# Optimization experiments

Hardware: AMD Instinct MI355X
Metric: run time of the kernel (lower is better)

## Reference

```python
import jax, jax.numpy as jnp
import numpy as np

L, E, K, H, I = 2, 8, 2, 1024, 2048  # stack_size, num_experts, top_k, hidden, intermediate
B, S = 1, 2048


def setup_inputs() -> dict:
    key = jax.random.key(0)
    k0, k1, k2, k3 = jax.random.split(key, 4)
    hidden_states = jax.random.normal(k0, (B, S, H), dtype=jnp.float32)
    router_w = jax.random.normal(k1, (L, H, E), dtype=jnp.float32) * 0.02
    gate_up_proj = jax.random.normal(k2, (L, E, H, 2 * I), dtype=jnp.float32) * (1.0 / np.sqrt(H))
    down_proj = jax.random.normal(k3, (L, E, I, H), dtype=jnp.float32) * (1.0 / np.sqrt(I))
    return {"hidden_states": hidden_states, "router_w": router_w,
            "gate_up_proj": gate_up_proj, "down_proj": down_proj}


def _moe_layer(x, rw, gu_w, dn_w):
    # x: [T,H]; one MoE block: RouterTopK(softmax) + full-capacity top-k GLU expert MLPs
    logits = x @ rw                                   # [T,E] router linear (fp32)
    aff = jax.nn.softmax(logits, axis=-1)
    vals, idx = jax.lax.top_k(aff, K)                 # [T,K]
    vals = vals / jnp.sum(vals, axis=-1, keepdims=True)  # normalize_top_k_affinities=True
    T = x.shape[0]
    # sparse combine weights [T,E]: normalized affinity on chosen experts, 0 elsewhere
    combine = jnp.zeros((T, E), x.dtype).at[jnp.arange(T)[:, None], idx].set(vals)
    gu = jnp.einsum('th,ehi->eti', x, gu_w)           # [E,T,2I] fused gate+up per expert
    gate, up = gu[..., :I], gu[..., I:]
    act = jax.nn.silu(gate) * up                      # GLU with silu
    eo = jnp.einsum('eti,eih->eth', act, dn_w)        # [E,T,H] down proj
    out = jnp.einsum('eth,te->th', eo, combine)       # combine over experts
    return out, logits


def reference(hidden_states, router_w, gate_up_proj, down_proj):
    Bx, Sx, Hx = hidden_states.shape
    x = hidden_states.reshape(-1, Hx)                 # [T,H]
    logits_all = []
    for l in range(L):                                # fixed small stack of layers
        x, logits = _moe_layer(x, router_w[l], gate_up_proj[l], down_proj[l])
        logits_all.append(logits)
    return x.reshape(Bx, Sx, Hx), jnp.stack(logits_all)  # output, [L,T,E] router logits
```

## Files before the change

kernel.cpp:

```cpp
#include <hip/hip_runtime.h>
#include <cstdint>
#include <cstddef>

constexpr int Lc = 2, Ec = 8, Hc = 1024, Ic = 2048, Tc = 2048;

typedef __bf16 bf16x8 __attribute__((ext_vector_type(8)));
typedef float f32x4 __attribute__((ext_vector_type(4)));

__device__ __forceinline__ unsigned short f2bf(float f) {
  unsigned u = __builtin_bit_cast(unsigned, f);
  u = (u + 0x7fffu + ((u >> 16) & 1u)) >> 16;
  return (unsigned short)u;
}
__device__ __forceinline__ float bf2f(unsigned short h) {
  unsigned u = (unsigned)h << 16;
  return __builtin_bit_cast(float, u);
}
__device__ __forceinline__ bf16x8 ldfrag(const unsigned short* p) {
  return __builtin_bit_cast(bf16x8, *(const uint4*)p);
}
__device__ __forceinline__ void gl2lds(const unsigned short* g, void* lds) {
  __builtin_amdgcn_global_load_lds(
      (const __attribute__((address_space(1))) void*)g,
      (__attribute__((address_space(3))) void*)lds, 16, 0, 0);
}

__global__ __launch_bounds__(256) void router_kernel(
    const float* __restrict__ x, const float* __restrict__ rw, float* __restrict__ logits,
    unsigned short* __restrict__ xh, unsigned short* __restrict__ xl) {
  const int t = blockIdx.x;
  const int tid = threadIdx.x;
  const float* xr = x + (size_t)t * Hc;
  const int h0 = tid * 4;
  const float4 v = *(const float4*)(xr + h0);
  const float f[4] = {v.x, v.y, v.z, v.w};
  unsigned short hs[4], ls[4];
#pragma unroll
  for (int j = 0; j < 4; ++j) {
    hs[j] = f2bf(f[j]);
    ls[j] = f2bf(f[j] - bf2f(hs[j]));
  }
  *(uint2*)(xh + (size_t)t * Hc + h0) =
      uint2{(unsigned)hs[0] | ((unsigned)hs[1] << 16), (unsigned)hs[2] | ((unsigned)hs[3] << 16)};
  *(uint2*)(xl + (size_t)t * Hc + h0) =
      uint2{(unsigned)ls[0] | ((unsigned)ls[1] << 16), (unsigned)ls[2] | ((unsigned)ls[3] << 16)};

  float acc[Ec];
#pragma unroll
  for (int e = 0; e < Ec; ++e) acc[e] = 0.f;
#pragma unroll
  for (int j = 0; j < 4; ++j) {
    const float* w = rw + (size_t)(h0 + j) * Ec;
#pragma unroll
    for (int e = 0; e < Ec; ++e) acc[e] += f[j] * w[e];
  }
  __shared__ float red[256][Ec];
#pragma unroll
  for (int e = 0; e < Ec; ++e) red[tid][e] = acc[e];
  __syncthreads();
  for (int s = 128; s > 0; s >>= 1) {
    if (tid < s) {
#pragma unroll
      for (int e = 0; e < Ec; ++e) red[tid][e] += red[tid + s][e];
    }
    __syncthreads();
  }
  if (tid < Ec) logits[(size_t)t * Ec + tid] = red[0][tid];
}

__global__ void topk_kernel(const float* __restrict__ logits, int* __restrict__ cnt,
                            int* __restrict__ tokList, float* __restrict__ wList) {
  const int t = blockIdx.x * blockDim.x + threadIdx.x;
  if (t >= Tc) return;
  float l[Ec];
#pragma unroll
  for (int e = 0; e < Ec; ++e) l[e] = logits[(size_t)t * Ec + e];
  float b0 = -3.4e38f, b1 = -3.4e38f;
  int i0 = 0, i1 = 0;
#pragma unroll
  for (int e = 0; e < Ec; ++e) {
    if (l[e] > b0) { b1 = b0; i1 = i0; b0 = l[e]; i0 = e; }
    else if (l[e] > b1) { b1 = l[e]; i1 = e; }
  }
  const float w0 = 1.f / (1.f + expf(b1 - b0));
  const float w1 = 1.f - w0;
  int p0 = atomicAdd(&cnt[i0], 1);
  tokList[i0 * Tc + p0] = t;
  wList[i0 * Tc + p0] = w0;
  int p1 = atomicAdd(&cnt[i1], 1);
  tokList[i1 * Tc + p1] = t;
  wList[i1 * Tc + p1] = w1;
}

__global__ void offsets_kernel(const int* __restrict__ cnt, int* __restrict__ off) {
  if (threadIdx.x == 0) {
    int s = 0;
    for (int e = 0; e < Ec; ++e) { off[e] = s; s += cnt[e]; }
  }
}

template <bool SPLIT>
__global__ __launch_bounds__(256) void wconv_kernel(const float* __restrict__ src,
                                                    unsigned short* __restrict__ dh,
                                                    unsigned short* __restrict__ dl,
                                                    int K, int N) {
  const int e = blockIdx.z;
  const int n0 = blockIdx.x * 64;
  const int k0 = blockIdx.y * 64;
  const int NB = N >> 6, KS = K >> 5;
  src += (size_t)e * K * N;

  __shared__ unsigned short lh[64][66];
  __shared__ unsigned short ll[SPLIT ? 64 : 1][66];
  const int tid = threadIdx.x;

  {
    const int r = tid >> 2, cg = (tid & 3) * 16;
    const float* sp = src + (size_t)(k0 + r) * N + n0 + cg;
#pragma unroll
    for (int i = 0; i < 16; i += 4) {
      const float4 v = *(const float4*)(sp + i);
      const float f[4] = {v.x, v.y, v.z, v.w};
#pragma unroll
      for (int j = 0; j < 4; ++j) {
        const unsigned short h = f2bf(f[j]);
        lh[r][cg + i + j] = h;
        if constexpr (SPLIT) ll[r][cg + i + j] = f2bf(f[j] - bf2f(h));
      }
    }
  }
  __syncthreads();
  {
    const int ksl = tid >> 7, q = (tid >> 5) & 3, n2 = (tid & 31) * 2;
    const int kb = ksl * 32 + q * 8;
    union { unsigned short s[16]; uint4 u[2]; } oh, ol;
#pragma unroll
    for (int s = 0; s < 2; ++s)
#pragma unroll
      for (int i = 0; i < 8; ++i) {
        oh.s[s * 8 + i] = lh[kb + i][n2 + s];
        if constexpr (SPLIT) ol.s[s * 8 + i] = ll[kb + i][n2 + s];
      }
    const size_t cb =
        (((size_t)e * NB + (n0 >> 6)) * KS + (k0 >> 5) + ksl) * 2048 + q * 512 + n2 * 8;
    *(uint4*)(dh + cb) = oh.u[0];
    *(uint4*)(dh + cb + 8) = oh.u[1];
    if constexpr (SPLIT) {
      *(uint4*)(dl + cb) = ol.u[0];
      *(uint4*)(dl + cb + 8) = ol.u[1];
    }
  }
}

template <bool SPLIT>
__global__ __launch_bounds__(256) void gateup_kernel(
    const unsigned short* __restrict__ xh, const unsigned short* __restrict__ xl,
    const unsigned short* __restrict__ gwSh, const unsigned short* __restrict__ gwSl,
    const int* __restrict__ cnt, const int* __restrict__ off,
    const int* __restrict__ tokList, unsigned short* __restrict__ actH,
    unsigned short* __restrict__ actL) {
  const int d = blockIdx.x;
  const int lid = (d & 7) * ((int)gridDim.x >> 3) + (d >> 3);
  const int mi = lid & 15;
  const int e = (lid >> 4) & 7;
  const int nb = lid >> 7;
  const int M = cnt[e];
  const int m0 = mi * 128;
  if (m0 >= M) return;
  const int tid = threadIdx.x;
  const int wv = tid >> 6, l64 = tid & 63;
  const int q = l64 >> 4, mr = l64 & 15;
  const int nc = wv * 16 + mr;
  const int wvo = wv * 1024;

  __shared__ __align__(16) unsigned short sBgh[3][2048];
  __shared__ __align__(16) unsigned short sBgl[3][SPLIT ? 2048 : 8];
  __shared__ __align__(16) unsigned short sBuh[3][2048];
  __shared__ __align__(16) unsigned short sBul[3][SPLIT ? 2048 : 8];
  __shared__ __align__(16) unsigned short sAh[2][128 * 40];
  __shared__ __align__(16) unsigned short sAl[2][SPLIT ? 128 * 40 : 8];

  const size_t gBase = (((size_t)e * 64 + nb) * 32) * 2048 + tid * 8;
  const size_t uBase = (((size_t)e * 64 + nb + 32) * 32) * 2048 + tid * 8;

  const int ar = tid >> 2, ak = (tid & 3) * 8;
  int r0 = m0 + ar;      if (r0 >= M) r0 = M - 1;
  int r1 = m0 + 64 + ar; if (r1 >= M) r1 = M - 1;
  const size_t a0o = (size_t)tokList[e * Tc + r0] * Hc + ak;
  const size_t a1o = (size_t)tokList[e * Tc + r1] * Hc + ak;

  f32x4 accg[8], accu[8];
#pragma unroll
  for (int i = 0; i < 8; ++i) {
    accg[i] = f32x4{0.f, 0.f, 0.f, 0.f};
    accu[i] = f32x4{0.f, 0.f, 0.f, 0.f};
  }

  uint4 pa0h{}, pa1h{}, pa0l{}, pa1l{};
  uint4 pb0h{}, pb1h{}, pb0l{}, pb1l{};

  pa0h = *(const uint4*)(xh + a0o);
  pa1h = *(const uint4*)(xh + a1o);
  if constexpr (SPLIT) {
    pa0l = *(const uint4*)(xl + a0o);
    pa1l = *(const uint4*)(xl + a1o);
  }
  gl2lds(gwSh + gBase, (char*)sBgh[0] + wvo);
  gl2lds(gwSh + uBase, (char*)sBuh[0] + wvo);
  if constexpr (SPLIT) {
    gl2lds(gwSl + gBase, (char*)sBgl[0] + wvo);
    gl2lds(gwSl + uBase, (char*)sBul[0] + wvo);
  }
  *(uint4*)&sAh[0][ar * 40 + ak] = pa0h;
  *(uint4*)&sAh[0][(ar + 64) * 40 + ak] = pa1h;
  if constexpr (SPLIT) {
    *(uint4*)&sAl[0][ar * 40 + ak] = pa0l;
    *(uint4*)&sAl[0][(ar + 64) * 40 + ak] = pa1l;
  }
  pa0h = *(const uint4*)(xh + a0o + 32);
  pa1h = *(const uint4*)(xh + a1o + 32);
  if constexpr (SPLIT) {
    pa0l = *(const uint4*)(xl + a0o + 32);
    pa1l = *(const uint4*)(xl + a1o + 32);
  }
  gl2lds(gwSh + gBase + 2048, (char*)sBgh[1] + wvo);
  gl2lds(gwSh + uBase + 2048, (char*)sBuh[1] + wvo);
  if constexpr (SPLIT) {
    gl2lds(gwSl + gBase + 2048, (char*)sBgl[1] + wvo);
    gl2lds(gwSl + uBase + 2048, (char*)sBul[1] + wvo);
  }
  if constexpr (SPLIT)
    asm volatile("s_waitcnt vmcnt(8) lgkmcnt(0)" ::: "memory");
  else
    asm volatile("s_waitcnt vmcnt(4) lgkmcnt(0)" ::: "memory");
  __builtin_amdgcn_s_barrier();
  __builtin_amdgcn_sched_barrier(0);

  int cbuf = 0, ibuf = 2;

#define GU_STEP(T, RB, WB, O0H, O1H, O0L, O1L, N0H, N1H, N0L, N1L)                      \
  {                                                                                     \
    if ((T) + 2 < 32) {                                                                 \
      N0H = *(const uint4*)(xh + a0o + ((T) + 2) * 32);                                 \
      N1H = *(const uint4*)(xh + a1o + ((T) + 2) * 32);                                 \
      if constexpr (SPLIT) {                                                            \
        N0L = *(const uint4*)(xl + a0o + ((T) + 2) * 32);                               \
        N1L = *(const uint4*)(xl + a1o + ((T) + 2) * 32);                               \
      }                                                                                 \
      gl2lds(gwSh + gBase + (size_t)((T) + 2) * 2048, (char*)sBgh[ibuf] + wvo);         \
      gl2lds(gwSh + uBase + (size_t)((T) + 2) * 2048, (char*)sBuh[ibuf] + wvo);         \
      if constexpr (SPLIT) {                                                            \
        gl2lds(gwSl + gBase + (size_t)((T) + 2) * 2048, (char*)sBgl[ibuf] + wvo);       \
        gl2lds(gwSl + uBase + (size_t)((T) + 2) * 2048, (char*)sBul[ibuf] + wvo);       \
      }                                                                                 \
    }                                                                                   \
    if ((T) + 1 < 32) {                                                                 \
      *(uint4*)&sAh[WB][ar * 40 + ak] = O0H;                                            \
      *(uint4*)&sAh[WB][(ar + 64) * 40 + ak] = O1H;                                     \
      if constexpr (SPLIT) {                                                            \
        *(uint4*)&sAl[WB][ar * 40 + ak] = O0L;                                          \
        *(uint4*)&sAl[WB][(ar + 64) * 40 + ak] = O1L;                                   \
      }                                                                                 \
    }                                                                                   \
    const bf16x8 bghf = ldfrag(&sBgh[cbuf][(q * 64 + nc) * 8]);                         \
    const bf16x8 buhf = ldfrag(&sBuh[cbuf][(q * 64 + nc) * 8]);                         \
    bf16x8 bglf, bulf;                                                                  \
    if constexpr (SPLIT) {                                                              \
      bglf = ldfrag(&sBgl[cbuf][(q * 64 + nc) * 8]);                                    \
      bulf = ldfrag(&sBul[cbuf][(q * 64 + nc) * 8]);                                    \
    }                                                                                   \
    _Pragma("unroll")                                                                   \
    for (int mt = 0; mt < 8; ++mt) {                                                    \
      const bf16x8 ah = ldfrag(&sAh[RB][(mt * 16 + mr) * 40 + q * 8]);                  \
      accg[mt] = __builtin_amdgcn_mfma_f32_16x16x32_bf16(ah, bghf, accg[mt], 0, 0, 0);  \
      accu[mt] = __builtin_amdgcn_mfma_f32_16x16x32_bf16(ah, buhf, accu[mt], 0, 0, 0);  \
      if constexpr (SPLIT) {                                                            \
        const bf16x8 alr = ldfrag(&sAl[RB][(mt * 16 + mr) * 40 + q * 8]);               \
        accg[mt] = __builtin_amdgcn_mfma_f32_16x16x32_bf16(ah, bglf, accg[mt], 0, 0, 0);\
        accg[mt] = __builtin_amdgcn_mfma_f32_16x16x32_bf16(alr, bghf, accg[mt], 0, 0, 0);\
        accu[mt] = __builtin_amdgcn_mfma_f32_16x16x32_bf16(ah, bulf, accu[mt], 0, 0, 0);\
        accu[mt] = __builtin_amdgcn_mfma_f32_16x16x32_bf16(alr, buhf, accu[mt], 0, 0, 0);\
      }                                                                                 \
    }                                                                                   \
    if ((T) < 31) {                                                                     \
      if ((T) + 2 < 32) {                                                               \
        if constexpr (SPLIT)                                                            \
          asm volatile("s_waitcnt vmcnt(8) lgkmcnt(0)" ::: "memory");                   \
        else                                                                            \
          asm volatile("s_waitcnt vmcnt(4) lgkmcnt(0)" ::: "memory");                   \
      } else {                                                                          \
        asm volatile("s_waitcnt vmcnt(0) lgkmcnt(0)" ::: "memory");                     \
      }                                                                                 \
      __builtin_amdgcn_s_barrier();                                                     \
      __builtin_amdgcn_sched_barrier(0);                                                \
    }                                                                                   \
    cbuf = cbuf == 2 ? 0 : cbuf + 1;                                                    \
    ibuf = ibuf == 2 ? 0 : ibuf + 1;                                                    \
  }

  for (int t = 0; t < 32; t += 2) {
    GU_STEP(t, 0, 1, pa0h, pa1h, pa0l, pa1l, pb0h, pb1h, pb0l, pb1l)
    GU_STEP(t + 1, 1, 0, pb0h, pb1h, pb0l, pb1l, pa0h, pa1h, pa0l, pa1l)
  }
#undef GU_STEP

  const int valid = M - m0;
  const int rowbase = off[e] + m0;
#pragma unroll
  for (int mt = 0; mt < 8; ++mt) {
#pragma unroll
    for (int r = 0; r < 4; ++r) {
      const int row = mt * 16 + q * 4 + r;
      if (row < valid) {
        const float g = accg[mt][r];
        const float u = accu[mt][r];
        const float a = (g / (1.f + expf(-g))) * u;
        const size_t idx = (size_t)(rowbase + row) * Ic + (nb * 64 + nc);
        const unsigned short h = f2bf(a);
        actH[idx] = h;
        if constexpr (SPLIT) actL[idx] = f2bf(a - bf2f(h));
      }
    }
  }
}

template <bool SPLIT>
__global__ __launch_bounds__(256) void down_kernel(
    const unsigned short* __restrict__ actH, const unsigned short* __restrict__ actL,
    const unsigned short* __restrict__ dwSh, const unsigned short* __restrict__ dwSl,
    const int* __restrict__ cnt, const int* __restrict__ off,
    const int* __restrict__ tokList, const float* __restrict__ wList,
    float* __restrict__ out) {
  const int d = blockIdx.x;
  const int lid = (d & 7) * ((int)gridDim.x >> 3) + (d >> 3);
  const int mi = lid & 15;
  const int e = (lid >> 4) & 7;
  const int nb = lid >> 7;
  const int M = cnt[e];
  const int m0 = mi * 128;
  if (m0 >= M) return;
  const int tid = threadIdx.x;
  const int wv = tid >> 6, l64 = tid & 63;
  const int q = l64 >> 4, mr = l64 & 15;
  const int nc = wv * 16 + mr;
  const int wvo = wv * 1024;

  __shared__ __align__(16) unsigned short sBh[3][2048];
  __shared__ __align__(16) unsigned short sBl[3][SPLIT ? 2048 : 8];
  __shared__ __align__(16) unsigned short sAh[2][128 * 40];
  __shared__ __align__(16) unsigned short sAl[2][SPLIT ? 128 * 40 : 8];
  __shared__ int sTok[128];
  __shared__ float sW[128];

  if (tid < 128) {
    int r = m0 + tid;
    int rc = r < M ? r : M - 1;
    sTok[tid] = tokList[e * Tc + rc];
    sW[tid] = wList[e * Tc + rc];
  }

  const size_t bBase = (((size_t)e * 16 + nb) * 64) * 2048 + tid * 8;
  const int offE = off[e];

  const int ar = tid >> 2, ak = (tid & 3) * 8;
  int r0 = m0 + ar;      if (r0 >= M) r0 = M - 1;
  int r1 = m0 + 64 + ar; if (r1 >= M) r1 = M - 1;
  const size_t a0o = (size_t)(offE + r0) * Ic + ak;
  const size_t a1o = (size_t)(offE + r1) * Ic + ak;

  f32x4 acc[8];
#pragma unroll
  for (int i = 0; i < 8; ++i) acc[i] = f32x4{0.f, 0.f, 0.f, 0.f};

  uint4 pa0h{}, pa1h{}, pa0l{}, pa1l{};
  uint4 pb0h{}, pb1h{}, pb0l{}, pb1l{};

  pa0h = *(const uint4*)(actH + a0o);
  pa1h = *(const uint4*)(actH + a1o);
  if constexpr (SPLIT) {
    pa0l = *(const uint4*)(actL + a0o);
    pa1l = *(const uint4*)(actL + a1o);
  }
  gl2lds(dwSh + bBase, (char*)sBh[0] + wvo);
  if constexpr (SPLIT) gl2lds(dwSl + bBase, (char*)sBl[0] + wvo);
  *(uint4*)&sAh[0][ar * 40 + ak] = pa0h;
  *(uint4*)&sAh[0][(ar + 64) * 40 + ak] = pa1h;
  if constexpr (SPLIT) {
    *(uint4*)&sAl[0][ar * 40 + ak] = pa0l;
    *(uint4*)&sAl[0][(ar + 64) * 40 + ak] = pa1l;
  }
  pa0h = *(const uint4*)(actH + a0o + 32);
  pa1h = *(const uint4*)(actH + a1o + 32);
  if constexpr (SPLIT) {
    pa0l = *(const uint4*)(actL + a0o + 32);
    pa1l = *(const uint4*)(actL + a1o + 32);
  }
  gl2lds(dwSh + bBase + 2048, (char*)sBh[1] + wvo);
  if constexpr (SPLIT) gl2lds(dwSl + bBase + 2048, (char*)sBl[1] + wvo);
  if constexpr (SPLIT)
    asm volatile("s_waitcnt vmcnt(6) lgkmcnt(0)" ::: "memory");
  else
    asm volatile("s_waitcnt vmcnt(3) lgkmcnt(0)" ::: "memory");
  __builtin_amdgcn_s_barrier();
  __builtin_amdgcn_sched_barrier(0);

  int cbuf = 0, ibuf = 2;

#define DN_STEP(T, RB, WB, O0H, O1H, O0L, O1L, N0H, N1H, N0L, N1L)                      \
  {                                                                                     \
    if ((T) + 2 < 64) {                                                                 \
      N0H = *(const uint4*)(actH + a0o + ((T) + 2) * 32);                               \
      N1H = *(const uint4*)(actH + a1o + ((T) + 2) * 32);                               \
      if constexpr (SPLIT) {                                                            \
        N0L = *(const uint4*)(actL + a0o + ((T) + 2) * 32);                             \
        N1L = *(const uint4*)(actL + a1o + ((T) + 2) * 32);                             \
      }                                                                                 \
      gl2lds(dwSh + bBase + (size_t)((T) + 2) * 2048, (char*)sBh[ibuf] + wvo);          \
      if constexpr (SPLIT)                                                              \
        gl2lds(dwSl + bBase + (size_t)((T) + 2) * 2048, (char*)sBl[ibuf] + wvo);        \
    }                                                                                   \
    if ((T) + 1 < 64) {                                                                 \
      *(uint4*)&sAh[WB][ar * 40 + ak] = O0H;                                            \
      *(uint4*)&sAh[WB][(ar + 64) * 40 + ak] = O1H;                                     \
      if constexpr (SPLIT) {                                                            \
        *(uint4*)&sAl[WB][ar * 40 + ak] = O0L;                                          \
        *(uint4*)&sAl[WB][(ar + 64) * 40 + ak] = O1L;                                   \
      }                                                                                 \
    }                                                                                   \
    const bf16x8 bh = ldfrag(&sBh[cbuf][(q * 64 + nc) * 8]);                            \
    bf16x8 bl;                                                                          \
    if constexpr (SPLIT) bl = ldfrag(&sBl[cbuf][(q * 64 + nc) * 8]);                    \
    _Pragma("unroll")                                                                   \
    for (int mt = 0; mt < 8; ++mt) {                                                    \
      const bf16x8 ah = ldfrag(&sAh[RB][(mt * 16 + mr) * 40 + q * 8]);                  \
      acc[mt] = __builtin_amdgcn_mfma_f32_16x16x32_bf16(ah, bh, acc[mt], 0, 0, 0);      \
      if constexpr (SPLIT) {                                                            \
        const bf16x8 alr = ldfrag(&sAl[RB][(mt * 16 + mr) * 40 + q * 8]);               \
        acc[mt] = __builtin_amdgcn_mfma_f32_16x16x32_bf16(ah, bl, acc[mt], 0, 0, 0);    \
        acc[mt] = __builtin_amdgcn_mfma_f32_16x16x32_bf16(alr, bh, acc[mt], 0, 0, 0);   \
      }                                                                                 \
    }                                                                                   \
    if ((T) < 63) {                                                                     \
      if ((T) + 2 < 64) {                                                               \
        if constexpr (SPLIT)                                                            \
          asm volatile("s_waitcnt vmcnt(6) lgkmcnt(0)" ::: "memory");                   \
        else                                                                            \
          asm volatile("s_waitcnt vmcnt(3) lgkmcnt(0)" ::: "memory");                   \
      } else {                                                                          \
        asm volatile("s_waitcnt vmcnt(0) lgkmcnt(0)" ::: "memory");                     \
      }                                                                                 \
      __builtin_amdgcn_s_barrier();                                                     \
      __builtin_amdgcn_sched_barrier(0);                                                \
    }                                                                                   \
    cbuf = cbuf == 2 ? 0 : cbuf + 1;                                                    \
    ibuf = ibuf == 2 ? 0 : ibuf + 1;                                                    \
  }

  for (int t = 0; t < 64; t += 2) {
    DN_STEP(t, 0, 1, pa0h, pa1h, pa0l, pa1l, pb0h, pb1h, pb0l, pb1l)
    DN_STEP(t + 1, 1, 0, pb0h, pb1h, pb0l, pb1l, pa0h, pa1h, pa0l, pa1l)
  }
#undef DN_STEP

  const int valid = M - m0;
#pragma unroll
  for (int mt = 0; mt < 8; ++mt) {
#pragma unroll
    for (int r = 0; r < 4; ++r) {
      const int row = mt * 16 + q * 4 + r;
      if (row < valid) {
        atomicAdd(&out[(size_t)sTok[row] * Hc + (nb * 64 + nc)], sW[row] * acc[mt][r]);
      }
    }
  }
}

extern "C" void kernel_launch(void* const* d_in, const int* in_sizes, int n_in, void* d_out,
                              int out_size, void* d_ws, size_t ws_size, hipStream_t stream) {
  const float* x_in = (const float*)d_in[0];
  const float* rw = (const float*)d_in[1];
  const float* guw = (const float*)d_in[2];
  const float* dnw = (const float*)d_in[3];
  float* out = (float*)d_out;
  float* logits_base = out + (size_t)Tc * Hc;

  uint8_t* w = (uint8_t*)d_ws;
  float* x1 = (float*)w;                    w += (size_t)Tc * Hc * 4;
  unsigned short* xh = (unsigned short*)w;  w += (size_t)Tc * Hc * 2;
  unsigned short* xl = (unsigned short*)w;  w += (size_t)Tc * Hc * 2;
  unsigned short* actH = (unsigned short*)w; w += (size_t)Tc * 2 * Ic * 2;
  unsigned short* actL = (unsigned short*)w; w += (size_t)Tc * 2 * Ic * 2;
  int* tokList = (int*)w;                   w += (size_t)Ec * Tc * 4;
  float* wList = (float*)w;                 w += (size_t)Ec * Tc * 4;
  int* cnt0 = (int*)w;                      w += 64;
  int* cnt1 = (int*)w;                      w += 64;
  int* off = (int*)w;                       w += 64;
  unsigned short* wTh = (unsigned short*)w; w += (size_t)Ec * 2 * Ic * Hc * 2;
  unsigned short* wTl = (unsigned short*)w; w += (size_t)Ec * 2 * Ic * Hc * 2;

  hipMemsetAsync(cnt0, 0, 192, stream);
  hipMemsetAsync(x1, 0, (size_t)Tc * Hc * 4, stream);
  hipMemsetAsync(out, 0, (size_t)Tc * Hc * 4, stream);

  router_kernel<<<Tc, 256, 0, stream>>>(x_in, rw, logits_base, xh, xl);
  topk_kernel<<<Tc / 256, 256, 0, stream>>>(logits_base, cnt0, tokList, wList);
  offsets_kernel<<<1, 64, 0, stream>>>(cnt0, off);
  wconv_kernel<true><<<dim3(2 * Ic / 64, Hc / 64, Ec), 256, 0, stream>>>(guw, wTh, wTl, Hc, 2 * Ic);
  gateup_kernel<true><<<16 * 32 * Ec, 256, 0, stream>>>(xh, xl, wTh, wTl, cnt0, off,
                                                        tokList, actH, actL);
  wconv_kernel<true><<<dim3(Hc / 64, Ic / 64, Ec), 256, 0, stream>>>(dnw, wTh, wTl, Ic, Hc);
  down_kernel<true><<<16 * 16 * Ec, 256, 0, stream>>>(actH, actL, wTh, wTl, cnt0,
                                                      off, tokList, wList, x1);

  const float* rw1 = rw + (size_t)Hc * Ec;
  const float* guw1 = guw + (size_t)Ec * Hc * 2 * Ic;
  const float* dnw1 = dnw + (size_t)Ec * Ic * Hc;
  router_kernel<<<Tc, 256, 0, stream>>>(x1, rw1, logits_base + (size_t)Tc * Ec, xh, xl);
  topk_kernel<<<Tc / 256, 256, 0, stream>>>(logits_base + (size_t)Tc * Ec, cnt1, tokList, wList);
  offsets_kernel<<<1, 64, 0, stream>>>(cnt1, off);
  wconv_kernel<false><<<dim3(2 * Ic / 64, Hc / 64, Ec), 256, 0, stream>>>(guw1, wTh, wTl, Hc, 2 * Ic);
  gateup_kernel<false><<<16 * 32 * Ec, 256, 0, stream>>>(xh, xl, wTh, wTl, cnt1, off,
                                                         tokList, actH, actL);
  wconv_kernel<false><<<dim3(Hc / 64, Ic / 64, Ec), 256, 0, stream>>>(dnw1, wTh, wTl, Ic, Hc);
  down_kernel<false><<<16 * 16 * Ec, 256, 0, stream>>>(actH, actL, wTh, wTl, cnt1,
                                                       off, tokList, wList, out);
}
```

Before: 1.066 ms.

## Load weight fragments directly into registers instead of staging through LDS

The gate-up and down expert GEMM kernels drop the triple-buffered LDS staging of B (weight) tiles via global_load_lds. Each lane now loads its own pre-swizzled weight fragment straight from global memory into registers, prefetched one k-step ahead. The kernels also add occupancy hints to launch_bounds and raise wave priority with s_setprio around the MFMA loop. This cuts LDS footprint and LDS read traffic to allow more resident blocks, at the risk of exposing global load latency with only one step of prefetch and adding register pressure.

```diff
diff --git a/kernel.cpp b/kernel.cpp
--- a/kernel.cpp
+++ b/kernel.cpp
@@ -18,11 +18,6 @@
 }
 __device__ __forceinline__ bf16x8 ldfrag(const unsigned short* p) {
   return __builtin_bit_cast(bf16x8, *(const uint4*)p);
-}
-__device__ __forceinline__ void gl2lds(const unsigned short* g, void* lds) {
-  __builtin_amdgcn_global_load_lds(
-      (const __attribute__((address_space(1))) void*)g,
-      (__attribute__((address_space(3))) void*)lds, 16, 0, 0);
 }
 
 __global__ __launch_bounds__(256) void router_kernel(
@@ -153,7 +148,7 @@
 }
 
 template <bool SPLIT>
-__global__ __launch_bounds__(256) void gateup_kernel(
+__global__ __launch_bounds__(256, SPLIT ? 3 : 4) void gateup_kernel(
     const unsigned short* __restrict__ xh, const unsigned short* __restrict__ xl,
     const unsigned short* __restrict__ gwSh, const unsigned short* __restrict__ gwSl,
     const int* __restrict__ cnt, const int* __restrict__ off,
@@ -171,17 +166,13 @@
   const int wv = tid >> 6, l64 = tid & 63;
   const int q = l64 >> 4, mr = l64 & 15;
   const int nc = wv * 16 + mr;
-  const int wvo = wv * 1024;
-
-  __shared__ __align__(16) unsigned short sBgh[3][2048];
-  __shared__ __align__(16) unsigned short sBgl[3][SPLIT ? 2048 : 8];
-  __shared__ __align__(16) unsigned short sBuh[3][2048];
-  __shared__ __align__(16) unsigned short sBul[3][SPLIT ? 2048 : 8];
+
   __shared__ __align__(16) unsigned short sAh[2][128 * 40];
   __shared__ __align__(16) unsigned short sAl[2][SPLIT ? 128 * 40 : 8];
 
-  const size_t gBase = (((size_t)e * 64 + nb) * 32) * 2048 + tid * 8;
-  const size_t uBase = (((size_t)e * 64 + nb + 32) * 32) * 2048 + tid * 8;
+  const size_t fragoff = (size_t)(q * 64 + nc) * 8;
+  const size_t gBase = (((size_t)e * 64 + nb) * 32) * 2048 + fragoff;
+  const size_t uBase = (((size_t)e * 64 + nb + 32) * 32) * 2048 + fragoff;
 
   const int ar = tid >> 2, ak = (tid & 3) * 8;
   int r0 = m0 + ar;      if (r0 >= M) r0 = M - 1;
@@ -196,111 +187,91 @@
     accu[i] = f32x4{0.f, 0.f, 0.f, 0.f};
   }
 
-  uint4 pa0h{}, pa1h{}, pa0l{}, pa1l{};
-  uint4 pb0h{}, pb1h{}, pb0l{}, pb1l{};
-
-  pa0h = *(const uint4*)(xh + a0o);
-  pa1h = *(const uint4*)(xh + a1o);
-  if constexpr (SPLIT) {
-    pa0l = *(const uint4*)(xl + a0o);
-    pa1l = *(const uint4*)(xl + a1o);
-  }
-  gl2lds(gwSh + gBase, (char*)sBgh[0] + wvo);
-  gl2lds(gwSh + uBase, (char*)sBuh[0] + wvo);
-  if constexpr (SPLIT) {
-    gl2lds(gwSl + gBase, (char*)sBgl[0] + wvo);
-    gl2lds(gwSl + uBase, (char*)sBul[0] + wvo);
-  }
-  *(uint4*)&sAh[0][ar * 40 + ak] = pa0h;
-  *(uint4*)&sAh[0][(ar + 64) * 40 + ak] = pa1h;
-  if constexpr (SPLIT) {
-    *(uint4*)&sAl[0][ar * 40 + ak] = pa0l;
-    *(uint4*)&sAl[0][(ar + 64) * 40 + ak] = pa1l;
-  }
-  pa0h = *(const uint4*)(xh + a0o + 32);
-  pa1h = *(const uint4*)(xh + a1o + 32);
-  if constexpr (SPLIT) {
-    pa0l = *(const uint4*)(xl + a0o + 32);
-    pa1l = *(const uint4*)(xl + a1o + 32);
-  }
-  gl2lds(gwSh + gBase + 2048, (char*)sBgh[1] + wvo);
-  gl2lds(gwSh + uBase + 2048, (char*)sBuh[1] + wvo);
-  if constexpr (SPLIT) {
-    gl2lds(gwSl + gBase + 2048, (char*)sBgl[1] + wvo);
-    gl2lds(gwSl + uBase + 2048, (char*)sBul[1] + wvo);
-  }
-  if constexpr (SPLIT)
-    asm volatile("s_waitcnt vmcnt(8) lgkmcnt(0)" ::: "memory");
-  else
-    asm volatile("s_waitcnt vmcnt(4) lgkmcnt(0)" ::: "memory");
+  uint4 paA0h{}, paA1h{}, paA0l{}, paA1l{};
+  uint4 paB0h{}, paB1h{}, paB0l{}, paB1l{};
+  bf16x8 bcAgh{}, bcAuh{}, bcAgl{}, bcAul{};
+  bf16x8 bcBgh{}, bcBuh{}, bcBgl{}, bcBul{};
+
+  paA0h = *(const uint4*)(xh + a0o);
+  paA1h = *(const uint4*)(xh + a1o);
+  if constexpr (SPLIT) {
+    paA0l = *(const uint4*)(xl + a0o);
+    paA1l = *(const uint4*)(xl + a1o);
+  }
+  *(uint4*)&sAh[0][ar * 40 + ak] = paA0h;
+  *(uint4*)&sAh[0][(ar + 64) * 40 + ak] = paA1h;
+  if constexpr (SPLIT) {
+    *(uint4*)&sAl[0][ar * 40 + ak] = paA0l;
+    *(uint4*)&sAl[0][(ar + 64) * 40 + ak] = paA1l;
+  }
+  bcAgh = ldfrag(gwSh + gBase);
+  bcAuh = ldfrag(gwSh + uBase);
+  if constexpr (SPLIT) {
+    bcAgl = ldfrag(gwSl + gBase);
+    bcAul = ldfrag(gwSl + uBase);
+  }
+  paA0h = *(const uint4*)(xh + a0o + 32);
+  paA1h = *(const uint4*)(xh + a1o + 32);
+  if constexpr (SPLIT) {
+    paA0l = *(const uint4*)(xl + a0o + 32);
+    paA1l = *(const uint4*)(xl + a1o + 32);
+  }
+  asm volatile("s_waitcnt lgkmcnt(0)" ::: "memory");
   __builtin_amdgcn_s_barrier();
-  __builtin_amdgcn_sched_barrier(0);
-
-  int cbuf = 0, ibuf = 2;
-
-#define GU_STEP(T, RB, WB, O0H, O1H, O0L, O1L, N0H, N1H, N0L, N1L)                      \
+
+#define GU_STEP(T, CUR, NX, PA0H, PA1H, PA0L, PA1L, PN0H, PN1H, PN0L, PN1L,             \
+                BCGH, BCUH, BCGL, BCUL, BNGH, BNUH, BNGL, BNUL)                         \
   {                                                                                     \
+    if ((T) + 1 < 32) {                                                                 \
+      BNGH = ldfrag(gwSh + gBase + (size_t)((T) + 1) * 2048);                           \
+      BNUH = ldfrag(gwSh + uBase + (size_t)((T) + 1) * 2048);                           \
+      if constexpr (SPLIT) {                                                            \
+        BNGL = ldfrag(gwSl + gBase + (size_t)((T) + 1) * 2048);                         \
+        BNUL = ldfrag(gwSl + uBase + (size_t)((T) + 1) * 2048);                         \
+      }                                                                                 \
+    }                                                                                   \
     if ((T) + 2 < 32) {                                                                 \
-      N0H = *(const uint4*)(xh + a0o + ((T) + 2) * 32);                                 \
-      N1H = *(const uint4*)(xh + a1o + ((T) + 2) * 32);                                 \
-      if constexpr (SPLIT) {                                                            \
-        N0L = *(const uint4*)(xl + a0o + ((T) + 2) * 32);                               \
-        N1L = *(const uint4*)(xl + a1o + ((T) + 2) * 32);                               \
-      }                                                                                 \
-      gl2lds(gwSh + gBase + (size_t)((T) + 2) * 2048, (char*)sBgh[ibuf] + wvo);         \
-      gl2lds(gwSh + uBase + (size_t)((T) + 2) * 2048, (char*)sBuh[ibuf] + wvo);         \
-      if constexpr (SPLIT) {                                                            \
-        gl2lds(gwSl + gBase + (size_t)((T) + 2) * 2048, (char*)sBgl[ibuf] + wvo);       \
-        gl2lds(gwSl + uBase + (size_t)((T) + 2) * 2048, (char*)sBul[ibuf] + wvo);       \
+      PN0H = *(const uint4*)(xh + a0o + ((T) + 2) * 32);                                \
+      PN1H = *(const uint4*)(xh + a1o + ((T) + 2) * 32);                                \
+      if constexpr (SPLIT) {                                                            \
+        PN0L = *(const uint4*)(xl + a0o + ((T) + 2) * 32);                              \
+        PN1L = *(const uint4*)(xl + a1o + ((T) + 2) * 32);                              \
       }                                                                                 \
     }                                                                                   \
     if ((T) + 1 < 32) {                                                                 \
-      *(uint4*)&sAh[WB][ar * 40 + ak] = O0H;                                            \
-      *(uint4*)&sAh[WB][(ar + 64) * 40 + ak] = O1H;                                     \
-      if constexpr (SPLIT) {                                                            \
-        *(uint4*)&sAl[WB][ar * 40 + ak] = O0L;                                          \
-        *(uint4*)&sAl[WB][(ar + 64) * 40 + ak] = O1L;                                   \
-      }                                                                                 \
-    }                                                                                   \
-    const bf16x8 bghf = ldfrag(&sBgh[cbuf][(q * 64 + nc) * 8]);                         \
-    const bf16x8 buhf = ldfrag(&sBuh[cbuf][(q * 64 + nc) * 8]);                         \
-    bf16x8 bglf, bulf;                                                                  \
-    if constexpr (SPLIT) {                                                              \
-      bglf = ldfrag(&sBgl[cbuf][(q * 64 + nc) * 8]);                                    \
-      bulf = ldfrag(&sBul[cbuf][(q * 64 + nc) * 8]);                                    \
-    }                                                                                   \
+      *(uint4*)&sAh[NX][ar * 40 + ak] = PA0H;                                           \
+      *(uint4*)&sAh[NX][(ar + 64) * 40 + ak] = PA1H;                                    \
+      if constexpr (SPLIT) {                                                            \
+        *(uint4*)&sAl[NX][ar * 40 + ak] = PA0L;                                         \
+        *(uint4*)&sAl[NX][(ar + 64) * 40 + ak] = PA1L;                                  \
+      }                                                                                 \
+    }                                                                                   \
+    __builtin_amdgcn_s_setprio(1);                                                      \
     _Pragma("unroll")                                                                   \
     for (int mt = 0; mt < 8; ++mt) {                                                    \
-      const bf16x8 ah = ldfrag(&sAh[RB][(mt * 16 + mr) * 40 + q * 8]);                  \
-      accg[mt] = __builtin_amdgcn_mfma_f32_16x16x32_bf16(ah, bghf, accg[mt], 0, 0, 0);  \
-      accu[mt] = __builtin_amdgcn_mfma_f32_16x16x32_bf16(ah, buhf, accu[mt], 0, 0, 0);  \
-      if constexpr (SPLIT) {                                                            \
-        const bf16x8 alr = ldfrag(&sAl[RB][(mt * 16 + mr) * 40 + q * 8]);               \
-        accg[mt] = __builtin_amdgcn_mfma_f32_16x16x32_bf16(ah, bglf, accg[mt], 0, 0, 0);\
-        accg[mt] = __builtin_amdgcn_mfma_f32_16x16x32_bf16(alr, bghf, accg[mt], 0, 0, 0);\
-        accu[mt] = __builtin_amdgcn_mfma_f32_16x16x32_bf16(ah, bulf, accu[mt], 0, 0, 0);\
-        accu[mt] = __builtin_amdgcn_mfma_f32_16x16x32_bf16(alr, buhf, accu[mt], 0, 0, 0);\
-      }                                                                                 \
-    }                                                                                   \
+      const bf16x8 ah = ldfrag(&sAh[CUR][(mt * 16 + mr) * 40 + q * 8]);                 \
+      accg[mt] = __builtin_amdgcn_mfma_f32_16x16x32_bf16(ah, BCGH, accg[mt], 0, 0, 0);  \
+      accu[mt] = __builtin_amdgcn_mfma_f32_16x16x32_bf16(ah, BCUH, accu[mt], 0, 0, 0);  \
+      if constexpr (SPLIT) {                                                            \
+        const bf16x8 alr = ldfrag(&sAl[CUR][(mt * 16 + mr) * 40 + q * 8]);              \
+        accg[mt] = __builtin_amdgcn_mfma_f32_16x16x32_bf16(ah, BCGL, accg[mt], 0, 0, 0);\
+        accg[mt] = __builtin_amdgcn_mfma_f32_16x16x32_bf16(alr, BCGH, accg[mt], 0, 0, 0);\
+        accu[mt] = __builtin_amdgcn_mfma_f32_16x16x32_bf16(ah, BCUL, accu[mt], 0, 0, 0);\
+        accu[mt] = __builtin_amdgcn_mfma_f32_16x16x32_bf16(alr, BCUH, accu[mt], 0, 0, 0);\
+      }                                                                                 \
+    }                                                                                   \
+    __builtin_amdgcn_s_setprio(0);                                                      \
     if ((T) < 31) {                                                                     \
-      if ((T) + 2 < 32) {                                                               \
-        if constexpr (SPLIT)                                                            \
-          asm volatile("s_waitcnt vmcnt(8) lgkmcnt(0)" ::: "memory");                   \
-        else                                                                            \
-          asm volatile("s_waitcnt vmcnt(4) lgkmcnt(0)" ::: "memory");                   \
-      } else {                                                                          \
-        asm volatile("s_waitcnt vmcnt(0) lgkmcnt(0)" ::: "memory");                     \
-      }                                                                                 \
+      asm volatile("s_waitcnt lgkmcnt(0)" ::: "memory");                                \
       __builtin_amdgcn_s_barrier();                                                     \
-      __builtin_amdgcn_sched_barrier(0);                                                \
-    }                                                                                   \
-    cbuf = cbuf == 2 ? 0 : cbuf + 1;                                                    \
-    ibuf = ibuf == 2 ? 0 : ibuf + 1;                                                    \
+    }                                                                                   \
   }
 
   for (int t = 0; t < 32; t += 2) {
-    GU_STEP(t, 0, 1, pa0h, pa1h, pa0l, pa1l, pb0h, pb1h, pb0l, pb1l)
-    GU_STEP(t + 1, 1, 0, pb0h, pb1h, pb0l, pb1l, pa0h, pa1h, pa0l, pa1l)
+    GU_STEP(t, 0, 1, paA0h, paA1h, paA0l, paA1l, paB0h, paB1h, paB0l, paB1l,
+            bcAgh, bcAuh, bcAgl, bcAul, bcBgh, bcBuh, bcBgl, bcBul)
+    GU_STEP(t + 1, 1, 0, paB0h, paB1h, paB0l, paB1l, paA0h, paA1h, paA0l, paA1l,
+            bcBgh, bcBuh, bcBgl, bcBul, bcAgh, bcAuh, bcAgl, bcAul)
   }
 #undef GU_STEP
 
@@ -325,7 +296,7 @@
 }
 
 template <bool SPLIT>
-__global__ __launch_bounds__(256) void down_kernel(
+__global__ __launch_bounds__(256, 4) void down_kernel(
     const unsigned short* __restrict__ actH, const unsigned short* __restrict__ actL,
     const unsigned short* __restrict__ dwSh, const unsigned short* __restrict__ dwSl,
     const int* __restrict__ cnt, const int* __restrict__ off,
@@ -343,10 +314,7 @@
   const int wv = tid >> 6, l64 = tid & 63;
   const int q = l64 >> 4, mr = l64 & 15;
   const int nc = wv * 16 + mr;
-  const int wvo = wv * 1024;
-
-  __shared__ __align__(16) unsigned short sBh[3][2048];
-  __shared__ __align__(16) unsigned short sBl[3][SPLIT ? 2048 : 8];
+
   __shared__ __align__(16) unsigned short sAh[2][128 * 40];
   __shared__ __align__(16) unsigned short sAl[2][SPLIT ? 128 * 40 : 8];
   __shared__ int sTok[128];
@@ -359,7 +327,8 @@
     sW[tid] = wList[e * Tc + rc];
   }
 
-  const size_t bBase = (((size_t)e * 16 + nb) * 64) * 2048 + tid * 8;
+  const size_t fragoff = (size_t)(q * 64 + nc) * 8;
+  const size_t bBase = (((size_t)e * 16 + nb) * 64) * 2048 + fragoff;
   const int offE = off[e];
 
   const int ar = tid >> 2, ak = (tid & 3) * 8;
@@ -372,93 +341,79 @@
 #pragma unroll
   for (int i = 0; i < 8; ++i) acc[i] = f32x4{0.f, 0.f, 0.f, 0.f};
 
-  uint4 pa0h{}, pa1h{}, pa0l{}, pa1l{};
-  uint4 pb0h{}, pb1h{}, pb0l{}, pb1l{};
-
-  pa0h = *(const uint4*)(actH + a0o);
-  pa1h = *(const uint4*)(actH + a1o);
-  if constexpr (SPLIT) {
-    pa0l = *(const uint4*)(actL + a0o);
-    pa1l = *(const uint4*)(actL + a1o);
-  }
-  gl2lds(dwSh + bBase, (char*)sBh[0] + wvo);
-  if constexpr (SPLIT) gl2lds(dwSl + bBase, (char*)sBl[0] + wvo);
-  *(uint4*)&sAh[0][ar * 40 + ak] = pa0h;
-  *(uint4*)&sAh[0][(ar + 64) * 40 + ak] = pa1h;
-  if constexpr (SPLIT) {
-    *(uint4*)&sAl[0][ar * 40 + ak] = pa0l;
-    *(uint4*)&sAl[0][(ar + 64) * 40 + ak] = pa1l;
-  }
-  pa0h = *(const uint4*)(actH + a0o + 32);
-  pa1h = *(const uint4*)(actH + a1o + 32);
-  if constexpr (SPLIT) {
-    pa0l = *(const uint4*)(actL + a0o + 32);
-    pa1l = *(const uint4*)(actL + a1o + 32);
-  }
-  gl2lds(dwSh + bBase + 2048, (char*)sBh[1] + wvo);
-  if constexpr (SPLIT) gl2lds(dwSl + bBase + 2048, (char*)sBl[1] + wvo);
-  if constexpr (SPLIT)
-    asm volatile("s_waitcnt vmcnt(6) lgkmcnt(0)" ::: "memory");
-  else
-    asm volatile("s_waitcnt vmcnt(3) lgkmcnt(0)" ::: "memory");
+  uint4 paA0h{}, paA1h{}, paA0l{}, paA1l{};
+  uint4 paB0h{}, paB1h{}, paB0l{}, paB1l{};
+  bf16x8 bcAh{}, bcAl{}, bcBh{}, bcBl{};
+
+  paA0h = *(const uint4*)(actH + a0o);
+  paA1h = *(const uint4*)(actH + a1o);
+  if constexpr (SPLIT) {
+    paA0l = *(const uint4*)(actL + a0o);
+    paA1l = *(const uint4*)(actL + a1o);
+  }
+  *(uint4*)&sAh[0][ar * 40 + ak] = paA0h;
+  *(uint4*)&sAh[0][(ar + 64) * 40 + ak] = paA1h;
+  if constexpr (SPLIT) {
+    *(uint4*)&sAl[0][ar * 40 + ak] = paA0l;
+    *(uint4*)&sAl[0][(ar + 64) * 40 + ak] = paA1l;
+  }
+  bcAh = ldfrag(dwSh + bBase);
+  if constexpr (SPLIT) bcAl = ldfrag(dwSl + bBase);
+  paA0h = *(const uint4*)(actH + a0o + 32);
+  paA1h = *(const uint4*)(actH + a1o + 32);
+  if constexpr (SPLIT) {
+    paA0l = *(const uint4*)(actL + a0o + 32);
+    paA1l = *(const uint4*)(actL + a1o + 32);
+  }
+  asm volatile("s_waitcnt lgkmcnt(0)" ::: "memory");
   __builtin_amdgcn_s_barrier();
-  __builtin_amdgcn_sched_barrier(0);
-
-  int cbuf = 0, ibuf = 2;
-
-#define DN_STEP(T, RB, WB, O0H, O1H, O0L, O1L, N0H, N1H, N0L, N1L)                      \
+
+#define DN_STEP(T, CUR, NX, PA0H, PA1H, PA0L, PA1L, PN0H, PN1H, PN0L, PN1L,             \
+                BCH, BCL, BNH, BNL)                                                     \
   {                                                                                     \
+    if ((T) + 1 < 64) {                                                                 \
+      BNH = ldfrag(dwSh + bBase + (size_t)((T) + 1) * 2048);                            \
+      if constexpr (SPLIT) BNL = ldfrag(dwSl + bBase + (size_t)((T) + 1) * 2048);       \
+    }                                                                                   \
     if ((T) + 2 < 64) {                                                                 \
-      N0H = *(const uint4*)(actH + a0o + ((T) + 2) * 32);                               \
-      N1H = *(const uint4*)(actH + a1o + ((T) + 2) * 32);                               \
-      if constexpr (SPLIT) {                                                            \
-        N0L = *(const uint4*)(actL + a0o + ((T) + 2) * 32);                             \
-        N1L = *(const uint4*)(actL + a1o + ((T) + 2) * 32);                             \
-      }                                                                                 \
-      gl2lds(dwSh + bBase + (size_t)((T) + 2) * 2048, (char*)sBh[ibuf] + wvo);          \
-      if constexpr (SPLIT)                                                              \
-        gl2lds(dwSl + bBase + (size_t)((T) + 2) * 2048, (char*)sBl[ibuf] + wvo);        \
+      PN0H = *(const uint4*)(actH + a0o + ((T) + 2) * 32);                              \
+      PN1H = *(const uint4*)(actH + a1o + ((T) + 2) * 32);                              \
+      if constexpr (SPLIT) {                                                            \
+        PN0L = *(const uint4*)(actL + a0o + ((T) + 2) * 32);                            \
+        PN1L = *(const uint4*)(actL + a1o + ((T) + 2) * 32);                            \
+      }                                                                                 \
     }                                                                                   \
     if ((T) + 1 < 64) {                                                                 \
-      *(uint4*)&sAh[WB][ar * 40 + ak] = O0H;                                            \
-      *(uint4*)&sAh[WB][(ar + 64) * 40 + ak] = O1H;                                     \
-      if constexpr (SPLIT) {                                                            \
-        *(uint4*)&sAl[WB][ar * 40 + ak] = O0L;                                          \
-        *(uint4*)&sAl[WB][(ar + 64) * 40 + ak] = O1L;                                   \
-      }                                                                                 \
-    }                                                                                   \
-    const bf16x8 bh = ldfrag(&sBh[cbuf][(q * 64 + nc) * 8]);                            \
-    bf16x8 bl;                                                                          \
-    if constexpr (SPLIT) bl = ldfrag(&sBl[cbuf][(q * 64 + nc) * 8]);                    \
+      *(uint4*)&sAh[NX][ar * 40 + ak] = PA0H;                                           \
+      *(uint4*)&sAh[NX][(ar + 64) * 40 + ak] = PA1H;                                    \
+      if constexpr (SPLIT) {                                                            \
+        *(uint4*)&sAl[NX][ar * 40 + ak] = PA0L;                                         \
+        *(uint4*)&sAl[NX][(ar + 64) * 40 + ak] = PA1L;                                  \
+      }                                                                                 \
+    }                                                                                   \
+    __builtin_amdgcn_s_setprio(1);                                                      \
     _Pragma("unroll")                                                                   \
     for (int mt = 0; mt < 8; ++mt) {                                                    \
-      const bf16x8 ah = ldfrag(&sAh[RB][(mt * 16 + mr) * 40 + q * 8]);                  \
-      acc[mt] = __builtin_amdgcn_mfma_f32_16x16x32_bf16(ah, bh, acc[mt], 0, 0, 0);      \
-      if constexpr (SPLIT) {                                                            \
-        const bf16x8 alr = ldfrag(&sAl[RB][(mt * 16 + mr) * 40 + q * 8]);               \
-        acc[mt] = __builtin_amdgcn_mfma_f32_16x16x32_bf16(ah, bl, acc[mt], 0, 0, 0);    \
-        acc[mt] = __builtin_amdgcn_mfma_f32_16x16x32_bf16(alr, bh, acc[mt], 0, 0, 0);   \
-      }                                                                                 \
-    }                                                                                   \
+      const bf16x8 ah = ldfrag(&sAh[CUR][(mt * 16 + mr) * 40 + q * 8]);                 \
+      acc[mt] = __builtin_amdgcn_mfma_f32_16x16x32_bf16(ah, BCH, acc[mt], 0, 0, 0);     \
+      if constexpr (SPLIT) {                                                            \
+        const bf16x8 alr = ldfrag(&sAl[CUR][(mt * 16 + mr) * 40 + q * 8]);              \
+        acc[mt] = __builtin_amdgcn_mfma_f32_16x16x32_bf16(ah, BCL, acc[mt], 0, 0, 0);   \
+        acc[mt] = __builtin_amdgcn_mfma_f32_16x16x32_bf16(alr, BCH, acc[mt], 0, 0, 0);  \
+      }                                                                                 \
+    }                                                                                   \
+    __builtin_amdgcn_s_setprio(0);                                                      \
     if ((T) < 63) {                                                                     \
-      if ((T) + 2 < 64) {                                                               \
-        if constexpr (SPLIT)                                                            \
-          asm volatile("s_waitcnt vmcnt(6) lgkmcnt(0)" ::: "memory");                   \
-        else                                                                            \
-          asm volatile("s_waitcnt vmcnt(3) lgkmcnt(0)" ::: "memory");                   \
-      } else {                                                                          \
-        asm volatile("s_waitcnt vmcnt(0) lgkmcnt(0)" ::: "memory");                     \
-      }                                                                                 \
+      asm volatile("s_waitcnt lgkmcnt(0)" ::: "memory");                                \
       __builtin_amdgcn_s_barrier();                                                     \
-      __builtin_amdgcn_sched_barrier(0);                                                \
-    }                                                                                   \
-    cbuf = cbuf == 2 ? 0 : cbuf + 1;                                                    \
-    ibuf = ibuf == 2 ? 0 : ibuf + 1;                                                    \
+    }                                                                                   \
   }
 
   for (int t = 0; t < 64; t += 2) {
-    DN_STEP(t, 0, 1, pa0h, pa1h, pa0l, pa1l, pb0h, pb1h, pb0l, pb1l)
-    DN_STEP(t + 1, 1, 0, pb0h, pb1h, pb0l, pb1l, pa0h, pa1h, pa0l, pa1l)
+    DN_STEP(t, 0, 1, paA0h, paA1h, paA0l, paA1l, paB0h, paB1h, paB0l, paB1l,
+            bcAh, bcAl, bcBh, bcBl)
+    DN_STEP(t + 1, 1, 0, paB0h, paB1h, paB0l, paB1l, paA0h, paA1h, paA0l, paA1l,
+            bcBh, bcBl, bcAh, bcAl)
   }
 #undef DN_STEP
 
```

Result: faster. 935.2 us (-12.3%).
